# Kernel tuning notes

Hardware: AMD Instinct MI355X
Metric: run time of the kernel (lower is better)

Reference implementation:

```python
import jax, jax.numpy as jnp
import numpy as np

N_USERS, N_ITEMS, NNZ = 16384, 8192, 1000000


def setup_inputs() -> dict:
    key = jax.random.key(0)
    k1, k2, k3 = jax.random.split(key, 3)
    values = jax.random.uniform(k1, (NNZ,), dtype=jnp.float32)
    rows = jnp.sort(jax.random.randint(k2, (NNZ,), 0, N_USERS, dtype=jnp.int32))
    cols = jax.random.randint(k3, (NNZ,), 0, N_ITEMS, dtype=jnp.int32)
    return {"values": values, "rows": rows, "cols": cols,
            "n_users": N_USERS, "n_items": N_ITEMS}


def _segment_softmax_if_positive(v, seg, num_segments):
    # torch code: softmax over a user's values only if their sum > 0, else raw.
    seg_sum = jax.ops.segment_sum(v, seg, num_segments=num_segments)
    apply_sm = seg_sum[seg] > 0
    seg_max = jax.ops.segment_max(v, seg, num_segments=num_segments)
    e = jnp.exp(v - seg_max[seg])
    denom = jax.ops.segment_sum(e, seg, num_segments=num_segments)
    return jnp.where(apply_sm, e / denom[seg], v)


def reference(values, rows, cols, n_users, n_items):
    # Densify sparse user-item matrix (coalesce: duplicates summed)
    R = jnp.zeros((n_users, n_items), dtype=values.dtype).at[rows, cols].add(values)
    # Level-1 Haar DWT + IDWT with only approx (popular) or only detail (niche):
    #   popular[2k] = popular[2k+1] = (x[2k]+x[2k+1])/2
    #   niche[2k]   = (x[2k]-x[2k+1])/2,  niche[2k+1] = -niche[2k]
    xe, xo = R[:, 0::2], R[:, 1::2]          # [U, I/2]
    avg = 0.5 * (xe + xo)
    diff = 0.5 * (xe - xo)
    half = cols // 2
    pop_v = avg[rows, half]
    sign = jnp.where(cols % 2 == 0, 1.0, -1.0).astype(values.dtype)
    nic_v = diff[rows, half] * sign
    uipg_vals = _segment_softmax_if_positive(pop_v, rows, n_users)
    uing_vals = _segment_softmax_if_positive(nic_v, rows, n_users)
    return jnp.stack([uipg_vals, uing_vals])  # [2, nnz]
```

## Files before the change

### kernel.cpp

```cpp
#include <hip/hip_runtime.h>


#define SEG_CAP 192
#define ROWS_PER_BLOCK 4

__global__ void build_row_ptr(const int* __restrict__ rows, int nnz, int n_users,
                              int* __restrict__ row_ptr) {
    const int i = blockIdx.x * blockDim.x + threadIdx.x;
    if (i > nnz) return;
    const int cur  = (i < nnz) ? rows[i] : n_users;
    const int prev = (i == 0) ? -1 : rows[i - 1];
    for (int r = prev + 1; r <= cur; ++r) row_ptr[r] = i;
}

__global__ __launch_bounds__(256) void uig_main(
    const float* __restrict__ values,
    const int*   __restrict__ cols,
    const int*   __restrict__ row_ptr,
    int nnz,
    float* __restrict__ out)
{
    const int wid  = threadIdx.x >> 6;
    const int lane = threadIdx.x & 63;
    const int r    = blockIdx.x * ROWS_PER_BLOCK + wid;

    __shared__ int    s_col[ROWS_PER_BLOCK][SEG_CAP];
    __shared__ float2 s_v[ROWS_PER_BLOCK][SEG_CAP];

    const int start = row_ptr[r];
    const int end   = row_ptr[r + 1];
    int k = end - start;
    if (k > SEG_CAP) k = SEG_CAP;

    for (int i = lane; i < k; i += 64) {
        const int   c = cols[start + i];
        const float v = values[start + i];
        s_col[wid][i] = c;
        s_v[wid][i]   = make_float2(v, (c & 1) ? -v : v);
    }
    __syncthreads();
    if (k <= 0) return;

    float pop_v[3], nic_v[3];
    float lsum_p = 0.f, lsum_n = 0.f, lmax_p = -INFINITY, lmax_n = -INFINITY;
    #pragma unroll
    for (int ii = 0; ii < 3; ++ii) {
        const int i = lane + ii * 64;
        pop_v[ii] = 0.f;
        nic_v[ii] = 0.f;
        if (i < k) {
            const int ci = s_col[wid][i];
            float S = 0.f, T = 0.f;
            for (int j = 0; j < k; ++j) {
                const int    cj = s_col[wid][j];
                const float2 vj = s_v[wid][j];
                const bool m = (((ci ^ cj) >> 1) == 0);
                S += m ? vj.x : 0.f;
                T += m ? vj.y : 0.f;
            }
            const float si = (ci & 1) ? -0.5f : 0.5f;
            pop_v[ii] = 0.5f * S;
            nic_v[ii] = si * T;
            lsum_p += pop_v[ii]; lmax_p = fmaxf(lmax_p, pop_v[ii]);
            lsum_n += nic_v[ii]; lmax_n = fmaxf(lmax_n, nic_v[ii]);
        }
    }

    #pragma unroll
    for (int off = 32; off >= 1; off >>= 1) {
        lsum_p += __shfl_xor(lsum_p, off);
        lsum_n += __shfl_xor(lsum_n, off);
        lmax_p  = fmaxf(lmax_p, __shfl_xor(lmax_p, off));
        lmax_n  = fmaxf(lmax_n, __shfl_xor(lmax_n, off));
    }

    float lde_p = 0.f, lde_n = 0.f;
    #pragma unroll
    for (int ii = 0; ii < 3; ++ii) {
        const int i = lane + ii * 64;
        if (i < k) {
            lde_p += expf(pop_v[ii] - lmax_p);
            lde_n += expf(nic_v[ii] - lmax_n);
        }
    }
    #pragma unroll
    for (int off = 32; off >= 1; off >>= 1) {
        lde_p += __shfl_xor(lde_p, off);
        lde_n += __shfl_xor(lde_n, off);
    }

    const bool ap = lsum_p > 0.f;
    const bool an = lsum_n > 0.f;

    #pragma unroll
    for (int ii = 0; ii < 3; ++ii) {
        const int i = lane + ii * 64;
        if (i < k) {
            const float op = ap ? (expf(pop_v[ii] - lmax_p) / lde_p) : pop_v[ii];
            const float on = an ? (expf(nic_v[ii] - lmax_n) / lde_n) : nic_v[ii];
            out[start + i]       = op;
            out[nnz + start + i] = on;
        }
    }
}

extern "C" void kernel_launch(void* const* d_in, const int* in_sizes, int n_in,
                              void* d_out, int out_size, void* d_ws, size_t ws_size,
                              hipStream_t stream) {
    const float* values = (const float*)d_in[0];
    const int*   rows   = (const int*)d_in[1];
    const int*   cols   = (const int*)d_in[2];
    const int nnz     = in_sizes[0];
    const int n_users = 16384;

    int* row_ptr = (int*)d_ws;
    float* out = (float*)d_out;

    build_row_ptr<<<(nnz + 1 + 255) / 256, 256, 0, stream>>>(rows, nnz, n_users, row_ptr);
    uig_main<<<n_users / ROWS_PER_BLOCK, 256, 0, stream>>>(values, cols, row_ptr, nnz, out);
}
```

Before: 92.15 us.

## Drop softmax max pass, pack shared entries, specialize rows up to 64 entries

```diff
diff --git a/kernel.cpp b/kernel.cpp
--- a/kernel.cpp
+++ b/kernel.cpp
@@ -1,8 +1,8 @@
 #include <hip/hip_runtime.h>
 
 
-#define SEG_CAP 192
-#define ROWS_PER_BLOCK 4
+#define SEG_CAP 128
+#define RPB 4
 
 __global__ void build_row_ptr(const int* __restrict__ rows, int nnz, int n_users,
                               int* __restrict__ row_ptr) {
@@ -22,85 +22,84 @@
 {
     const int wid  = threadIdx.x >> 6;
     const int lane = threadIdx.x & 63;
-    const int r    = blockIdx.x * ROWS_PER_BLOCK + wid;
+    const int r    = blockIdx.x * RPB + wid;
 
-    __shared__ int    s_col[ROWS_PER_BLOCK][SEG_CAP];
-    __shared__ float2 s_v[ROWS_PER_BLOCK][SEG_CAP];
+    __shared__ float4 s_e[RPB][SEG_CAP];
 
     const int start = row_ptr[r];
-    const int end   = row_ptr[r + 1];
-    int k = end - start;
+    int k = row_ptr[r + 1] - start;
     if (k > SEG_CAP) k = SEG_CAP;
 
-    for (int i = lane; i < k; i += 64) {
-        const int   c = cols[start + i];
-        const float v = values[start + i];
-        s_col[wid][i] = c;
-        s_v[wid][i]   = make_float2(v, (c & 1) ? -v : v);
+    int   h0 = -1, h1 = -1;
+    float sg0 = 0.f, sg1 = 0.f;
+    if (lane < k) {
+        const int   c  = cols[start + lane];
+        const float hv = 0.5f * values[start + lane];
+        const float sv = (c & 1) ? -hv : hv;
+        h0 = c >> 1; sg0 = (c & 1) ? -1.f : 1.f;
+        s_e[wid][lane] = make_float4(__int_as_float(h0), hv, sv, 0.f);
+    }
+    if (lane + 64 < k) {
+        const int   c  = cols[start + lane + 64];
+        const float hv = 0.5f * values[start + lane + 64];
+        const float sv = (c & 1) ? -hv : hv;
+        h1 = c >> 1; sg1 = (c & 1) ? -1.f : 1.f;
+        s_e[wid][lane + 64] = make_float4(__int_as_float(h1), hv, sv, 0.f);
     }
     __syncthreads();
     if (k <= 0) return;
 
-    float pop_v[3], nic_v[3];
-    float lsum_p = 0.f, lsum_n = 0.f, lmax_p = -INFINITY, lmax_n = -INFINITY;
-    #pragma unroll
-    for (int ii = 0; ii < 3; ++ii) {
-        const int i = lane + ii * 64;
-        pop_v[ii] = 0.f;
-        nic_v[ii] = 0.f;
-        if (i < k) {
-            const int ci = s_col[wid][i];
-            float S = 0.f, T = 0.f;
-            for (int j = 0; j < k; ++j) {
-                const int    cj = s_col[wid][j];
-                const float2 vj = s_v[wid][j];
-                const bool m = (((ci ^ cj) >> 1) == 0);
-                S += m ? vj.x : 0.f;
-                T += m ? vj.y : 0.f;
-            }
-            const float si = (ci & 1) ? -0.5f : 0.5f;
-            pop_v[ii] = 0.5f * S;
-            nic_v[ii] = si * T;
-            lsum_p += pop_v[ii]; lmax_p = fmaxf(lmax_p, pop_v[ii]);
-            lsum_n += nic_v[ii]; lmax_n = fmaxf(lmax_n, nic_v[ii]);
+    float S0 = 0.f, T0 = 0.f, S1 = 0.f, T1 = 0.f;
+    if (k <= 64) {
+        for (int j = 0; j < k; ++j) {
+            const float4 e = s_e[wid][j];
+            const bool m0 = (__float_as_int(e.x) == h0);
+            S0 += m0 ? e.y : 0.f;
+            T0 += m0 ? e.z : 0.f;
+        }
+    } else {
+        for (int j = 0; j < k; ++j) {
+            const float4 e  = s_e[wid][j];
+            const int    hj = __float_as_int(e.x);
+            const bool m0 = (hj == h0);
+            const bool m1 = (hj == h1);
+            S0 += m0 ? e.y : 0.f;
+            T0 += m0 ? e.z : 0.f;
+            S1 += m1 ? e.y : 0.f;
+            T1 += m1 ? e.z : 0.f;
         }
     }
+    const float pop0 = S0, nic0 = sg0 * T0;
+    const float pop1 = S1, nic1 = sg1 * T1;
 
+    const bool a0 = (lane < k), a1 = (lane + 64 < k);
+    const float e_p0 = expf(pop0), e_n0 = expf(nic0);
+    const float e_p1 = expf(pop1), e_n1 = expf(nic1);
+
+    float sum_p = (a0 ? pop0 : 0.f) + (a1 ? pop1 : 0.f);
+    float sum_n = (a0 ? nic0 : 0.f) + (a1 ? nic1 : 0.f);
+    float de_p  = (a0 ? e_p0 : 0.f) + (a1 ? e_p1 : 0.f);
+    float de_n  = (a0 ? e_n0 : 0.f) + (a1 ? e_n1 : 0.f);
     #pragma unroll
     for (int off = 32; off >= 1; off >>= 1) {
-        lsum_p += __shfl_xor(lsum_p, off);
-        lsum_n += __shfl_xor(lsum_n, off);
-        lmax_p  = fmaxf(lmax_p, __shfl_xor(lmax_p, off));
-        lmax_n  = fmaxf(lmax_n, __shfl_xor(lmax_n, off));
+        sum_p += __shfl_xor(sum_p, off);
+        sum_n += __shfl_xor(sum_n, off);
+        de_p  += __shfl_xor(de_p,  off);
+        de_n  += __shfl_xor(de_n,  off);
     }
 
-    float lde_p = 0.f, lde_n = 0.f;
-    #pragma unroll
-    for (int ii = 0; ii < 3; ++ii) {
-        const int i = lane + ii * 64;
-        if (i < k) {
-            lde_p += expf(pop_v[ii] - lmax_p);
-            lde_n += expf(nic_v[ii] - lmax_n);
-        }
+    const bool  ap = sum_p > 0.f;
+    const bool  an = sum_n > 0.f;
+    const float rp = 1.0f / de_p;
+    const float rn = 1.0f / de_n;
+
+    if (a0) {
+        out[start + lane]       = ap ? e_p0 * rp : pop0;
+        out[nnz + start + lane] = an ? e_n0 * rn : nic0;
     }
-    #pragma unroll
-    for (int off = 32; off >= 1; off >>= 1) {
-        lde_p += __shfl_xor(lde_p, off);
-        lde_n += __shfl_xor(lde_n, off);
-    }
-
-    const bool ap = lsum_p > 0.f;
-    const bool an = lsum_n > 0.f;
-
-    #pragma unroll
-    for (int ii = 0; ii < 3; ++ii) {
-        const int i = lane + ii * 64;
-        if (i < k) {
-            const float op = ap ? (expf(pop_v[ii] - lmax_p) / lde_p) : pop_v[ii];
-            const float on = an ? (expf(nic_v[ii] - lmax_n) / lde_n) : nic_v[ii];
-            out[start + i]       = op;
-            out[nnz + start + i] = on;
-        }
+    if (a1) {
+        out[start + lane + 64]       = ap ? e_p1 * rp : pop1;
+        out[nnz + start + lane + 64] = an ? e_n1 * rn : nic1;
     }
 }
 
@@ -117,5 +116,5 @@
     float* out = (float*)d_out;
 
     build_row_ptr<<<(nnz + 1 + 255) / 256, 256, 0, stream>>>(rows, nnz, n_users, row_ptr);
-    uig_main<<<n_users / ROWS_PER_BLOCK, 256, 0, stream>>>(values, cols, row_ptr, nnz, out);
+    uig_main<<<n_users / RPB, 256, 0, stream>>>(values, cols, row_ptr, nnz, out);
 }
```

Result: no change. 92.09 us (-0.1%).
